# Kernel tuning notes

Measured on AMD Instinct MI355X. Metric: run time of the kernel, lower is better.

## Reference

```python
import jax, jax.numpy as jnp
import numpy as np

N_EMB = 768
HEAD_SIZE = 64
B, T = 256, 256


def setup_inputs() -> dict:
    key = jax.random.key(0)
    kx, kq, kk, kv = jax.random.split(key, 4)
    x = jax.random.normal(kx, (B, T, N_EMB), dtype=jnp.float32)
    # nn.Linear(n_emb, head_size, bias=False): store as [in, out], apply x @ W
    s = 1.0 / np.sqrt(N_EMB)
    Wq = jax.random.uniform(kq, (N_EMB, HEAD_SIZE), jnp.float32, -s, s)
    Wk = jax.random.uniform(kk, (N_EMB, HEAD_SIZE), jnp.float32, -s, s)
    Wv = jax.random.uniform(kv, (N_EMB, HEAD_SIZE), jnp.float32, -s, s)
    return {"x": x, "Wq": Wq, "Wk": Wk, "Wv": Wv}


def reference(x, Wq, Wk, Wv):
    # x: [B, T, C]
    q = x @ Wq  # [B, T, H]
    k = x @ Wk  # [B, T, H]
    v = x @ Wv  # [B, T, H]
    scale = k.shape[-1] ** (-0.5)
    wei = jnp.einsum('bth,bsh->bts', q, k) * scale  # [B, T, T]
    t = x.shape[1]
    causal = jnp.tril(jnp.ones((t, t), dtype=bool))  # [T, T]
    wei = jnp.where(causal, wei, -jnp.inf)
    wei = jax.nn.softmax(wei, axis=-1)
    out = jnp.einsum('bts,bsh->bth', wei, v)  # [B, T, H]
    return out
```

## Files before the change

kernel.cpp:

```cpp
#include <hip/hip_runtime.h>
#include <hip/hip_bf16.h>
#include <stdint.h>


typedef __attribute__((ext_vector_type(8))) short short8;
typedef __attribute__((ext_vector_type(4))) short short4v;
typedef __attribute__((ext_vector_type(4))) float f32x4;

#define MFMA16(a, b, c) __builtin_amdgcn_mfma_f32_16x16x32_bf16(a, b, c, 0, 0, 0)

static __device__ __forceinline__ unsigned short f2bf(float f) {
  union { float f; uint32_t u; } v; v.f = f;
  return (unsigned short)((v.u + 0x7FFFu + ((v.u >> 16) & 1u)) >> 16);
}

__global__ void wt_prep(const float* __restrict__ Wq, const float* __restrict__ Wk,
                        const float* __restrict__ Wv, unsigned short* __restrict__ Wt) {
  int idx = blockIdx.x * 256 + threadIdx.x;
  if (idx >= 192 * 768) return;
  int row = idx / 768;
  int k = idx - row * 768;
  int m = row >> 6, c = row & 63;
  const float* W = (m == 0) ? Wq : (m == 1 ? Wk : Wv);
  Wt[idx] = f2bf(W[k * 64 + c]);
}

#define XS0 0
#define XS1 20480
#define WS0 40960
#define WS1 56320
#define KOFF 71680
#define VOFF 104448

__global__ __launch_bounds__(512, 2) void fused_head(
    const float* __restrict__ x, const unsigned short* __restrict__ Wt,
    float* __restrict__ out) {
  __shared__ char smem[137216];
  const int tid = threadIdx.x;
  const int w = tid >> 6;
  const int lane = tid & 63;
  const int l15 = lane & 15, g = lane >> 4;
  const int b = blockIdx.x;
  const float* xb = x + (size_t)b * 256 * 768;

  f32x4 acc[2][12];
  #pragma unroll
  for (int rt = 0; rt < 2; ++rt)
    #pragma unroll
    for (int ct = 0; ct < 12; ++ct) acc[rt][ct] = f32x4{0.f, 0.f, 0.f, 0.f};

  const int sxr = tid >> 3;
  const int sxc = tid & 7;
  const int widx0 = tid;
  const int widx1 = 512 + tid;

  float4 xreg[4];
  short8 wreg[2];

  auto load_tiles = [&](int kk) {
    #pragma unroll
    for (int p = 0; p < 4; ++p)
      xreg[p] = *reinterpret_cast<const float4*>(
          xb + (size_t)(p * 64 + sxr) * 768 + kk + sxc * 4);
    wreg[0] = *reinterpret_cast<const short8*>(
        Wt + (size_t)(widx0 >> 2) * 768 + kk + (widx0 & 3) * 8);
    if (widx1 < 768)
      wreg[1] = *reinterpret_cast<const short8*>(
          Wt + (size_t)(widx1 >> 2) * 768 + kk + (widx1 & 3) * 8);
  };
  auto store_tiles = [&](char* xsb, char* wsb) {
    #pragma unroll
    for (int p = 0; p < 4; ++p) {
      short4v v;
      v[0] = (short)f2bf(xreg[p].x); v[1] = (short)f2bf(xreg[p].y);
      v[2] = (short)f2bf(xreg[p].z); v[3] = (short)f2bf(xreg[p].w);
      *reinterpret_cast<short4v*>(xsb + (p * 64 + sxr) * 80 + sxc * 8) = v;
    }
    *reinterpret_cast<short8*>(wsb + (widx0 >> 2) * 80 + (widx0 & 3) * 16) = wreg[0];
    if (widx1 < 768)
      *reinterpret_cast<short8*>(wsb + (widx1 >> 2) * 80 + (widx1 & 3) * 16) = wreg[1];
  };

  load_tiles(0);
  store_tiles(smem + XS0, smem + WS0);

  for (int it = 0; it < 24; ++it) {
    __syncthreads();
    const int cur = it & 1;
    if (it < 23) load_tiles((it + 1) * 32);
    char* xsb = smem + (cur ? XS1 : XS0);
    char* wsb = smem + (cur ? WS1 : WS0);
    short8 a0 = *reinterpret_cast<const short8*>(xsb + (w * 32 + l15) * 80 + g * 16);
    short8 a1 = *reinterpret_cast<const short8*>(xsb + (w * 32 + 16 + l15) * 80 + g * 16);
    #pragma unroll
    for (int ct = 0; ct < 12; ++ct) {
      short8 bb = *reinterpret_cast<const short8*>(wsb + (ct * 16 + l15) * 80 + g * 16);
      acc[0][ct] = MFMA16(a0, bb, acc[0][ct]);
      acc[1][ct] = MFMA16(a1, bb, acc[1][ct]);
    }
    if (it < 23) store_tiles(smem + (cur ? XS0 : XS1), smem + (cur ? WS0 : WS1));
  }
  __syncthreads();

  char* Kl = smem + KOFF;
  char* Vl = smem + VOFF;
  char* Ql = smem;
  #pragma unroll
  for (int rt = 0; rt < 2; ++rt) {
    #pragma unroll
    for (int ct = 0; ct < 4; ++ct) {
      #pragma unroll
      for (int r = 0; r < 4; ++r) {
        int key = w * 32 + rt * 16 + g * 4 + r;
        int h = ct * 16 + l15;
        *reinterpret_cast<unsigned short*>(
            Kl + key * 128 + ((h * 2) ^ ((key & 7) << 4))) = f2bf(acc[rt][4 + ct][r]);
        *reinterpret_cast<unsigned short*>(
            Ql + key * 256 + ((h * 2) ^ ((key & 15) << 4))) =
            f2bf(0.125f * acc[rt][ct][r]);
      }
      int h = ct * 16 + l15;
      int t0 = w * 32 + rt * 16 + g * 4;
      short4v pv;
      pv[0] = (short)f2bf(acc[rt][8 + ct][0]); pv[1] = (short)f2bf(acc[rt][8 + ct][1]);
      pv[2] = (short)f2bf(acc[rt][8 + ct][2]); pv[3] = (short)f2bf(acc[rt][8 + ct][3]);
      *reinterpret_cast<short4v*>(Vl + h * 512 + ((t0 * 2) ^ ((h & 7) << 4))) = pv;
    }
  }
  __syncthreads();

  short8 qf[2][2];
  #pragma unroll
  for (int rt = 0; rt < 2; ++rt)
    #pragma unroll
    for (int c = 0; c < 2; ++c) {
      int row = w * 32 + rt * 16 + l15;
      qf[rt][c] = *reinterpret_cast<const short8*>(
          Ql + row * 256 + ((c * 64 + g * 16) ^ ((row & 15) << 4)));
    }
  __syncthreads();

  char* Pw = smem + w * 8192;

  #pragma unroll
  for (int rt = 0; rt < 2; ++rt) {
    const int trow0 = w * 32 + rt * 16;
    const int ntile = (trow0 >> 4) + 1;
    f32x4 s[16];

    #pragma unroll
    for (int t = 0; t < 16; ++t) {
      if (t < ntile) {
        int key = t * 16 + l15;
        int swz = (l15 & 7) << 4;
        short8 b0 = *reinterpret_cast<const short8*>(Kl + key * 128 + ((g * 16) ^ swz));
        short8 b1 = *reinterpret_cast<const short8*>(Kl + key * 128 + ((64 + g * 16) ^ swz));
        f32x4 a = f32x4{0.f, 0.f, 0.f, 0.f};
        a = MFMA16(qf[rt][0], b0, a);
        a = MFMA16(qf[rt][1], b1, a);
        s[t] = a;
      }
    }

    float mx[4] = {-1e30f, -1e30f, -1e30f, -1e30f};
    #pragma unroll
    for (int t = 0; t < 16; ++t) {
      if (t < ntile) {
        if (t == ntile - 1) {
          #pragma unroll
          for (int r = 0; r < 4; ++r)
            if (l15 > g * 4 + r) s[t][r] = -1e30f;
        }
        #pragma unroll
        for (int r = 0; r < 4; ++r) mx[r] = fmaxf(mx[r], s[t][r]);
      }
    }
    #pragma unroll
    for (int r = 0; r < 4; ++r) {
      mx[r] = fmaxf(mx[r], __shfl_xor(mx[r], 1));
      mx[r] = fmaxf(mx[r], __shfl_xor(mx[r], 2));
      mx[r] = fmaxf(mx[r], __shfl_xor(mx[r], 4));
      mx[r] = fmaxf(mx[r], __shfl_xor(mx[r], 8));
    }
    float sm[4] = {0.f, 0.f, 0.f, 0.f};
    #pragma unroll
    for (int t = 0; t < 16; ++t) {
      if (t < ntile) {
        #pragma unroll
        for (int r = 0; r < 4; ++r) {
          float p = __expf(s[t][r] - mx[r]);
          s[t][r] = p;
          sm[r] += p;
        }
      }
    }
    float inv[4];
    #pragma unroll
    for (int r = 0; r < 4; ++r) {
      sm[r] += __shfl_xor(sm[r], 1);
      sm[r] += __shfl_xor(sm[r], 2);
      sm[r] += __shfl_xor(sm[r], 4);
      sm[r] += __shfl_xor(sm[r], 8);
      inv[r] = 1.0f / sm[r];
    }

    #pragma unroll
    for (int t = 0; t < 16; ++t) {
      if (t < ntile) {
        #pragma unroll
        for (int r = 0; r < 4; ++r) {
          int lrow = g * 4 + r;
          *reinterpret_cast<unsigned short*>(
              Pw + lrow * 512 + (((t * 16 + l15) * 2) ^ (lrow << 4))) =
              f2bf(s[t][r] * inv[r]);
        }
      }
    }
    if (ntile & 1) {
      #pragma unroll
      for (int r = 0; r < 4; ++r) {
        int lrow = g * 4 + r;
        *reinterpret_cast<unsigned short*>(
            Pw + lrow * 512 + (((ntile * 16 + l15) * 2) ^ (lrow << 4))) = 0;
      }
    }

    const int nkc = (ntile + 1) >> 1;
    f32x4 o[4];
    #pragma unroll
    for (int i = 0; i < 4; ++i) o[i] = f32x4{0.f, 0.f, 0.f, 0.f};
    #pragma unroll
    for (int kc = 0; kc < 8; ++kc) {
      if (kc < nkc) {
        short8 pa = *reinterpret_cast<const short8*>(
            Pw + l15 * 512 + ((kc * 64 + g * 16) ^ (l15 << 4)));
        #pragma unroll
        for (int ht = 0; ht < 4; ++ht) {
          int h = ht * 16 + l15;
          short8 bv = *reinterpret_cast<const short8*>(
              Vl + h * 512 + ((kc * 64 + g * 16) ^ ((h & 7) << 4)));
          o[ht] = MFMA16(pa, bv, o[ht]);
        }
      }
    }

    #pragma unroll
    for (int r = 0; r < 4; ++r) {
      int trow = trow0 + g * 4 + r;
      float* dst = out + ((size_t)b * 256 + trow) * 64 + l15;
      #pragma unroll
      for (int ht = 0; ht < 4; ++ht) dst[ht * 16] = o[ht][r];
    }
  }
}

extern "C" void kernel_launch(void* const* d_in, const int* in_sizes, int n_in,
                              void* d_out, int out_size, void* d_ws, size_t ws_size,
                              hipStream_t stream) {
  const float* x  = (const float*)d_in[0];
  const float* Wq = (const float*)d_in[1];
  const float* Wk = (const float*)d_in[2];
  const float* Wv = (const float*)d_in[3];
  unsigned short* Wt = (unsigned short*)d_ws;
  float* out = (float*)d_out;

  hipLaunchKernelGGL(wt_prep, dim3(576), dim3(256), 0, stream, Wq, Wk, Wv, Wt);
  hipLaunchKernelGGL(fused_head, dim3(256), dim3(512), 0, stream, x, Wt, out);
}
```

Before: 58.29 us.

## Load x directly into MFMA registers and pre-tile weights for LDS staging

The projection GEMM no longer stages x through shared memory. Each lane loads its own fp32 x fragment straight from global memory, converts it to bf16 in registers and feeds it to the MFMA, with a register double-buffer for the next K step. Weights are pre-laid out by the prep kernel in a padded per-K-tile order, so the block can copy each tile contiguously into LDS. This removes the x LDS writes and reads and the conversion store. In exchange, x loads are less coalesced (each lane reads 32 contiguous bytes from a different row) and the shared-memory allocation grows, which may limit occupancy.

```diff
diff --git a/kernel.cpp b/kernel.cpp
--- a/kernel.cpp
+++ b/kernel.cpp
@@ -14,34 +14,48 @@
   return (unsigned short)((v.u + 0x7FFFu + ((v.u >> 16) & 1u)) >> 16);
 }
 
+static __device__ __forceinline__ short8 conv8(float4 lo, float4 hi) {
+  short8 a;
+  a[0] = (short)f2bf(lo.x); a[1] = (short)f2bf(lo.y);
+  a[2] = (short)f2bf(lo.z); a[3] = (short)f2bf(lo.w);
+  a[4] = (short)f2bf(hi.x); a[5] = (short)f2bf(hi.y);
+  a[6] = (short)f2bf(hi.z); a[7] = (short)f2bf(hi.w);
+  return a;
+}
+
 __global__ void wt_prep(const float* __restrict__ Wq, const float* __restrict__ Wk,
-                        const float* __restrict__ Wv, unsigned short* __restrict__ Wt) {
+                        const float* __restrict__ Wv, unsigned short* __restrict__ WtT) {
   int idx = blockIdx.x * 256 + threadIdx.x;
-  if (idx >= 192 * 768) return;
-  int row = idx / 768;
-  int k = idx - row * 768;
-  int m = row >> 6, c = row & 63;
+  if (idx >= 147456) return;
+  int it = idx / 6144;
+  int rem = idx - it * 6144;
+  int r = rem >> 5, c = rem & 31;
+  int m = r >> 6, co = r & 63;
   const float* W = (m == 0) ? Wq : (m == 1 ? Wk : Wv);
-  Wt[idx] = f2bf(W[k * 64 + c]);
-}
-
-#define XS0 0
-#define XS1 20480
-#define WS0 40960
-#define WS1 56320
-#define KOFF 71680
-#define VOFF 104448
+  WtT[it * 7680 + r * 40 + c] = f2bf(W[(it * 32 + c) * 64 + co]);
+}
+
+#define WT0 65536
+#define WT1 80896
+#define KOFF 96256
+#define VOFF 129024
 
 __global__ __launch_bounds__(512, 2) void fused_head(
-    const float* __restrict__ x, const unsigned short* __restrict__ Wt,
+    const float* __restrict__ x, const unsigned short* __restrict__ WtT,
     float* __restrict__ out) {
-  __shared__ char smem[137216];
+  __shared__ char smem[161792];
   const int tid = threadIdx.x;
   const int w = tid >> 6;
   const int lane = tid & 63;
   const int l15 = lane & 15, g = lane >> 4;
   const int b = blockIdx.x;
-  const float* xb = x + (size_t)b * 256 * 768;
+  const float* xB = x + (size_t)b * 256 * 768;
+  const float* xp0 = xB + (size_t)(w * 32 + l15) * 768 + g * 8;
+  const float* xp1 = xp0 + 16 * 768;
+
+  char* wt0 = smem + WT0;
+  char* wt1 = smem + WT1;
+  const bool stv = (tid < 480);
 
   f32x4 acc[2][12];
   #pragma unroll
@@ -49,58 +63,74 @@
     #pragma unroll
     for (int ct = 0; ct < 12; ++ct) acc[rt][ct] = f32x4{0.f, 0.f, 0.f, 0.f};
 
-  const int sxr = tid >> 3;
-  const int sxc = tid & 7;
-  const int widx0 = tid;
-  const int widx1 = 512 + tid;
-
-  float4 xreg[4];
-  short8 wreg[2];
-
-  auto load_tiles = [&](int kk) {
-    #pragma unroll
-    for (int p = 0; p < 4; ++p)
-      xreg[p] = *reinterpret_cast<const float4*>(
-          xb + (size_t)(p * 64 + sxr) * 768 + kk + sxc * 4);
-    wreg[0] = *reinterpret_cast<const short8*>(
-        Wt + (size_t)(widx0 >> 2) * 768 + kk + (widx0 & 3) * 8);
-    if (widx1 < 768)
-      wreg[1] = *reinterpret_cast<const short8*>(
-          Wt + (size_t)(widx1 >> 2) * 768 + kk + (widx1 & 3) * 8);
-  };
-  auto store_tiles = [&](char* xsb, char* wsb) {
-    #pragma unroll
-    for (int p = 0; p < 4; ++p) {
-      short4v v;
-      v[0] = (short)f2bf(xreg[p].x); v[1] = (short)f2bf(xreg[p].y);
-      v[2] = (short)f2bf(xreg[p].z); v[3] = (short)f2bf(xreg[p].w);
-      *reinterpret_cast<short4v*>(xsb + (p * 64 + sxr) * 80 + sxc * 8) = v;
-    }
-    *reinterpret_cast<short8*>(wsb + (widx0 >> 2) * 80 + (widx0 & 3) * 16) = wreg[0];
-    if (widx1 < 768)
-      *reinterpret_cast<short8*>(wsb + (widx1 >> 2) * 80 + (widx1 & 3) * 16) = wreg[1];
-  };
-
-  load_tiles(0);
-  store_tiles(smem + XS0, smem + WS0);
-
-  for (int it = 0; it < 24; ++it) {
-    __syncthreads();
-    const int cur = it & 1;
-    if (it < 23) load_tiles((it + 1) * 32);
-    char* xsb = smem + (cur ? XS1 : XS0);
-    char* wsb = smem + (cur ? WS1 : WS0);
-    short8 a0 = *reinterpret_cast<const short8*>(xsb + (w * 32 + l15) * 80 + g * 16);
-    short8 a1 = *reinterpret_cast<const short8*>(xsb + (w * 32 + 16 + l15) * 80 + g * 16);
-    #pragma unroll
-    for (int ct = 0; ct < 12; ++ct) {
-      short8 bb = *reinterpret_cast<const short8*>(wsb + (ct * 16 + l15) * 80 + g * 16);
-      acc[0][ct] = MFMA16(a0, bb, acc[0][ct]);
-      acc[1][ct] = MFMA16(a1, bb, acc[1][ct]);
-    }
-    if (it < 23) store_tiles(smem + (cur ? XS0 : XS1), smem + (cur ? WS0 : WS1));
-  }
+  if (stv) {
+    const short8* s = reinterpret_cast<const short8*>(WtT + (size_t)tid * 16);
+    *reinterpret_cast<short8*>(wt0 + tid * 32) = s[0];
+    *reinterpret_cast<short8*>(wt0 + tid * 32 + 16) = s[1];
+  }
+  float4 A0 = *reinterpret_cast<const float4*>(xp0);
+  float4 A1 = *reinterpret_cast<const float4*>(xp0 + 4);
+  float4 A2 = *reinterpret_cast<const float4*>(xp1);
+  float4 A3 = *reinterpret_cast<const float4*>(xp1 + 4);
+  float4 B0, B1, B2, B3;
   __syncthreads();
+
+  for (int ito = 0; ito < 12; ++ito) {
+    const int it1 = 2 * ito + 1;
+    {
+      short8 wr0, wr1;
+      if (stv) {
+        const short8* s = reinterpret_cast<const short8*>(
+            WtT + (size_t)it1 * 7680 + tid * 16);
+        wr0 = s[0]; wr1 = s[1];
+      }
+      B0 = *reinterpret_cast<const float4*>(xp0 + it1 * 32);
+      B1 = *reinterpret_cast<const float4*>(xp0 + it1 * 32 + 4);
+      B2 = *reinterpret_cast<const float4*>(xp1 + it1 * 32);
+      B3 = *reinterpret_cast<const float4*>(xp1 + it1 * 32 + 4);
+      short8 a0 = conv8(A0, A1);
+      short8 a1 = conv8(A2, A3);
+      #pragma unroll
+      for (int ct = 0; ct < 12; ++ct) {
+        short8 bb = *reinterpret_cast<const short8*>(wt0 + (ct * 16 + l15) * 80 + g * 16);
+        acc[0][ct] = MFMA16(a0, bb, acc[0][ct]);
+        acc[1][ct] = MFMA16(a1, bb, acc[1][ct]);
+      }
+      if (stv) {
+        *reinterpret_cast<short8*>(wt1 + tid * 32) = wr0;
+        *reinterpret_cast<short8*>(wt1 + tid * 32 + 16) = wr1;
+      }
+      __syncthreads();
+    }
+    {
+      const bool pf = (ito < 11);
+      short8 wr0, wr1;
+      if (pf && stv) {
+        const short8* s = reinterpret_cast<const short8*>(
+            WtT + (size_t)(it1 + 1) * 7680 + tid * 16);
+        wr0 = s[0]; wr1 = s[1];
+      }
+      if (pf) {
+        A0 = *reinterpret_cast<const float4*>(xp0 + (it1 + 1) * 32);
+        A1 = *reinterpret_cast<const float4*>(xp0 + (it1 + 1) * 32 + 4);
+        A2 = *reinterpret_cast<const float4*>(xp1 + (it1 + 1) * 32);
+        A3 = *reinterpret_cast<const float4*>(xp1 + (it1 + 1) * 32 + 4);
+      }
+      short8 a0 = conv8(B0, B1);
+      short8 a1 = conv8(B2, B3);
+      #pragma unroll
+      for (int ct = 0; ct < 12; ++ct) {
+        short8 bb = *reinterpret_cast<const short8*>(wt1 + (ct * 16 + l15) * 80 + g * 16);
+        acc[0][ct] = MFMA16(a0, bb, acc[0][ct]);
+        acc[1][ct] = MFMA16(a1, bb, acc[1][ct]);
+      }
+      if (pf && stv) {
+        *reinterpret_cast<short8*>(wt0 + tid * 32) = wr0;
+        *reinterpret_cast<short8*>(wt0 + tid * 32 + 16) = wr1;
+      }
+      __syncthreads();
+    }
+  }
 
   char* Kl = smem + KOFF;
   char* Vl = smem + VOFF;
@@ -261,9 +291,9 @@
   const float* Wq = (const float*)d_in[1];
   const float* Wk = (const float*)d_in[2];
   const float* Wv = (const float*)d_in[3];
-  unsigned short* Wt = (unsigned short*)d_ws;
+  unsigned short* WtT = (unsigned short*)d_ws;
   float* out = (float*)d_out;
 
-  hipLaunchKernelGGL(wt_prep, dim3(576), dim3(256), 0, stream, Wq, Wk, Wv, Wt);
-  hipLaunchKernelGGL(fused_head, dim3(256), dim3(512), 0, stream, x, Wt, out);
-}
+  hipLaunchKernelGGL(wt_prep, dim3(576), dim3(256), 0, stream, Wq, Wk, Wv, WtT);
+  hipLaunchKernelGGL(fused_head, dim3(256), dim3(512), 0, stream, x, WtT, out);
+}
```

Result: slower. 62.35 us (+7.0%).

## Deepen projection prefetch pipeline and pre-tile weights for contiguous loads

Applied to the files above, without the earlier changes.

The QKV projection loop now keeps two register buffers of x and weight tiles in flight, prefetching two K-steps ahead instead of one. The loop is unrolled by two over ping-pong LDS buffers. The weight prep kernel writes weights already tiled and padded per K-step, so each thread does two contiguous 16-byte loads and LDS stores without index math. Barriers are replaced by a custom lgkmcnt wait plus s_barrier, and the barrier after the Q fragment read is dropped, which is safe because each warp only overwrites its own Q rows. This costs more registers and a larger shared-memory declaration, and aims to hide global-load latency in the memory-bound projection phase.

```diff
diff --git a/kernel.cpp b/kernel.cpp
--- a/kernel.cpp
+++ b/kernel.cpp
@@ -9,20 +9,26 @@
 
 #define MFMA16(a, b, c) __builtin_amdgcn_mfma_f32_16x16x32_bf16(a, b, c, 0, 0, 0)
 
+#define BAR() do { \
+  asm volatile("s_waitcnt lgkmcnt(0)" ::: "memory"); \
+  __builtin_amdgcn_s_barrier(); \
+} while (0)
+
 static __device__ __forceinline__ unsigned short f2bf(float f) {
   union { float f; uint32_t u; } v; v.f = f;
   return (unsigned short)((v.u + 0x7FFFu + ((v.u >> 16) & 1u)) >> 16);
 }
 
 __global__ void wt_prep(const float* __restrict__ Wq, const float* __restrict__ Wk,
-                        const float* __restrict__ Wv, unsigned short* __restrict__ Wt) {
+                        const float* __restrict__ Wv, unsigned short* __restrict__ WtT) {
   int idx = blockIdx.x * 256 + threadIdx.x;
-  if (idx >= 192 * 768) return;
-  int row = idx / 768;
-  int k = idx - row * 768;
-  int m = row >> 6, c = row & 63;
+  if (idx >= 147456) return;
+  int it = idx / 6144;
+  int rem = idx - it * 6144;
+  int r = rem >> 5, c = rem & 31;
+  int m = r >> 6, co = r & 63;
   const float* W = (m == 0) ? Wq : (m == 1 ? Wk : Wv);
-  Wt[idx] = f2bf(W[k * 64 + c]);
+  WtT[it * 7680 + r * 40 + c] = f2bf(W[(it * 32 + c) * 64 + co]);
 }
 
 #define XS0 0
@@ -33,15 +39,20 @@
 #define VOFF 104448
 
 __global__ __launch_bounds__(512, 2) void fused_head(
-    const float* __restrict__ x, const unsigned short* __restrict__ Wt,
+    const float* __restrict__ x, const unsigned short* __restrict__ WtT,
     float* __restrict__ out) {
-  __shared__ char smem[137216];
+  __shared__ char smem[161792];
   const int tid = threadIdx.x;
   const int w = tid >> 6;
   const int lane = tid & 63;
   const int l15 = lane & 15, g = lane >> 4;
   const int b = blockIdx.x;
-  const float* xb = x + (size_t)b * 256 * 768;
+  const float* xB = x + (size_t)b * 256 * 768;
+
+  char* xs0 = smem + XS0;
+  char* xs1 = smem + XS1;
+  char* ws0 = smem + WS0;
+  char* ws1 = smem + WS1;
 
   f32x4 acc[2][12];
   #pragma unroll
@@ -51,45 +62,39 @@
 
   const int sxr = tid >> 3;
   const int sxc = tid & 7;
-  const int widx0 = tid;
-  const int widx1 = 512 + tid;
-
-  float4 xreg[4];
-  short8 wreg[2];
-
-  auto load_tiles = [&](int kk) {
+  const bool stv = (tid < 480);
+
+  float4 xA[4], xPB[4];
+  short8 wA[2], wPB[2];
+
+  auto loadX = [&](float4* xr, int kk) {
     #pragma unroll
     for (int p = 0; p < 4; ++p)
-      xreg[p] = *reinterpret_cast<const float4*>(
-          xb + (size_t)(p * 64 + sxr) * 768 + kk + sxc * 4);
-    wreg[0] = *reinterpret_cast<const short8*>(
-        Wt + (size_t)(widx0 >> 2) * 768 + kk + (widx0 & 3) * 8);
-    if (widx1 < 768)
-      wreg[1] = *reinterpret_cast<const short8*>(
-          Wt + (size_t)(widx1 >> 2) * 768 + kk + (widx1 & 3) * 8);
-  };
-  auto store_tiles = [&](char* xsb, char* wsb) {
+      xr[p] = *reinterpret_cast<const float4*>(
+          xB + (size_t)(p * 64 + sxr) * 768 + kk + sxc * 4);
+  };
+  auto loadW = [&](short8* wr, int it) {
+    if (stv) {
+      const short8* s = reinterpret_cast<const short8*>(WtT + (size_t)it * 7680 + tid * 16);
+      wr[0] = s[0]; wr[1] = s[1];
+    }
+  };
+  auto storeX = [&](char* xsb, const float4* xr) {
     #pragma unroll
     for (int p = 0; p < 4; ++p) {
       short4v v;
-      v[0] = (short)f2bf(xreg[p].x); v[1] = (short)f2bf(xreg[p].y);
-      v[2] = (short)f2bf(xreg[p].z); v[3] = (short)f2bf(xreg[p].w);
+      v[0] = (short)f2bf(xr[p].x); v[1] = (short)f2bf(xr[p].y);
+      v[2] = (short)f2bf(xr[p].z); v[3] = (short)f2bf(xr[p].w);
       *reinterpret_cast<short4v*>(xsb + (p * 64 + sxr) * 80 + sxc * 8) = v;
     }
-    *reinterpret_cast<short8*>(wsb + (widx0 >> 2) * 80 + (widx0 & 3) * 16) = wreg[0];
-    if (widx1 < 768)
-      *reinterpret_cast<short8*>(wsb + (widx1 >> 2) * 80 + (widx1 & 3) * 16) = wreg[1];
-  };
-
-  load_tiles(0);
-  store_tiles(smem + XS0, smem + WS0);
-
-  for (int it = 0; it < 24; ++it) {
-    __syncthreads();
-    const int cur = it & 1;
-    if (it < 23) load_tiles((it + 1) * 32);
-    char* xsb = smem + (cur ? XS1 : XS0);
-    char* wsb = smem + (cur ? WS1 : WS0);
+  };
+  auto storeW = [&](char* wsb, const short8* wr) {
+    if (stv) {
+      *reinterpret_cast<short8*>(wsb + tid * 32) = wr[0];
+      *reinterpret_cast<short8*>(wsb + tid * 32 + 16) = wr[1];
+    }
+  };
+  auto compute = [&](const char* xsb, const char* wsb) {
     short8 a0 = *reinterpret_cast<const short8*>(xsb + (w * 32 + l15) * 80 + g * 16);
     short8 a1 = *reinterpret_cast<const short8*>(xsb + (w * 32 + 16 + l15) * 80 + g * 16);
     #pragma unroll
@@ -98,9 +103,23 @@
       acc[0][ct] = MFMA16(a0, bb, acc[0][ct]);
       acc[1][ct] = MFMA16(a1, bb, acc[1][ct]);
     }
-    if (it < 23) store_tiles(smem + (cur ? XS0 : XS1), smem + (cur ? WS0 : WS1));
+  };
+
+  loadX(xA, 0); loadW(wA, 0);
+  storeX(xs0, xA); storeW(ws0, wA);
+  loadX(xPB, 32); loadW(wPB, 1);
+  BAR();
+
+  for (int j = 0; j < 12; ++j) {
+    if (2 * j + 2 < 24) { loadX(xA, (2 * j + 2) * 32); loadW(wA, 2 * j + 2); }
+    compute(xs0, ws0);
+    storeX(xs1, xPB); storeW(ws1, wPB);
+    BAR();
+    if (2 * j + 3 < 24) { loadX(xPB, (2 * j + 3) * 32); loadW(wPB, 2 * j + 3); }
+    compute(xs1, ws1);
+    if (2 * j + 2 < 24) { storeX(xs0, xA); storeW(ws0, wA); }
+    BAR();
   }
-  __syncthreads();
 
   char* Kl = smem + KOFF;
   char* Vl = smem + VOFF;
@@ -127,7 +146,7 @@
       *reinterpret_cast<short4v*>(Vl + h * 512 + ((t0 * 2) ^ ((h & 7) << 4))) = pv;
     }
   }
-  __syncthreads();
+  BAR();
 
   short8 qf[2][2];
   #pragma unroll
@@ -138,7 +157,6 @@
       qf[rt][c] = *reinterpret_cast<const short8*>(
           Ql + row * 256 + ((c * 64 + g * 16) ^ ((row & 15) << 4)));
     }
-  __syncthreads();
 
   char* Pw = smem + w * 8192;
 
@@ -261,9 +279,9 @@
   const float* Wq = (const float*)d_in[1];
   const float* Wk = (const float*)d_in[2];
   const float* Wv = (const float*)d_in[3];
-  unsigned short* Wt = (unsigned short*)d_ws;
+  unsigned short* WtT = (unsigned short*)d_ws;
   float* out = (float*)d_out;
 
-  hipLaunchKernelGGL(wt_prep, dim3(576), dim3(256), 0, stream, Wq, Wk, Wv, Wt);
-  hipLaunchKernelGGL(fused_head, dim3(256), dim3(512), 0, stream, x, Wt, out);
-}
+  hipLaunchKernelGGL(wt_prep, dim3(576), dim3(256), 0, stream, Wq, Wk, Wv, WtT);
+  hipLaunchKernelGGL(fused_head, dim3(256), dim3(512), 0, stream, x, WtT, out);
+}
```

Result: faster. 53.26 us (-8.6%).
